# Performance work log

Hardware: AMD Instinct MI355X
Metric: run time of the kernel (lower is better)

The kernel has to match this reference:

```python
import jax, jax.numpy as jnp
import numpy as np

N = 100000
HEADS = 1
DIM = 64
NEG_SLOPE = 0.2


def gat_layer(x, src, dst, W, a_src, a_dst, b):
    # x: [N, F_in]; src/dst: [E] (edge j->i: src=j source, dst=i target)
    h = (x @ W).reshape(N, HEADS, DIM)                      # [N,H,D]
    al_s = jnp.sum(h * a_src[None, :, :], axis=-1)          # [N,H]
    al_d = jnp.sum(h * a_dst[None, :, :], axis=-1)          # [N,H]
    e = jax.nn.leaky_relu(al_s[src] + al_d[dst], NEG_SLOPE)  # [E,H]
    # per-destination softmax (scatter softmax)
    m = jax.ops.segment_max(e, dst, num_segments=N)          # [N,H]
    ex = jnp.exp(e - m[dst])
    s = jax.ops.segment_sum(ex, dst, num_segments=N)         # [N,H]
    alpha = ex / s[dst]                                      # [E,H]
    msg = alpha[:, :, None] * h[src]                         # [E,H,D]
    out = jax.ops.segment_sum(msg, dst, num_segments=N)      # [N,H,D]
    return out.reshape(N, HEADS * DIM) + b


def setup_inputs() -> dict:
    key = jax.random.key(0)
    ks = jax.random.split(key, 16)
    E = 1600000
    inp = {
        'x': jax.random.normal(ks[0], (N, 128), dtype=jnp.float32),
        'edge_index': jax.random.randint(ks[1], (2, E), 0, N, dtype=jnp.int64),
    }
    dims_in = [128, 64, 64]
    for i in range(3):
        fi = dims_in[i]
        inp[f'W{i}'] = jax.random.normal(ks[2 + 4 * i], (fi, HEADS * DIM), dtype=jnp.float32) / np.sqrt(fi)
        inp[f'as{i}'] = jax.random.normal(ks[3 + 4 * i], (HEADS, DIM), dtype=jnp.float32) / np.sqrt(DIM)
        inp[f'ad{i}'] = jax.random.normal(ks[4 + 4 * i], (HEADS, DIM), dtype=jnp.float32) / np.sqrt(DIM)
        inp[f'b{i}'] = jnp.zeros((HEADS * DIM,), dtype=jnp.float32)
    return inp


def reference(x, edge_index, W0, as0, ad0, b0, W1, as1, ad1, b1, W2, as2, ad2, b2):
    # add self-loops (PyG GATConv default add_self_loops=True)
    loop = jnp.arange(N, dtype=edge_index.dtype)
    src = jnp.concatenate([edge_index[0], loop])
    dst = jnp.concatenate([edge_index[1], loop])
    x = gat_layer(x, src, dst, W0, as0, ad0, b0)
    x = jax.nn.relu(x)
    x = gat_layer(x, src, dst, W1, as1, ad1, b1)
    x = jax.nn.relu(x)
    x = gat_layer(x, src, dst, W2, as2, ad2, b2)
    return x
```

## Files before the change

### kernel.cpp

```cpp
#include <hip/hip_runtime.h>
#include <hip/hip_fp16.h>
#include <math.h>

#define DIM 64
#define CBSH 9
#define CBSZ (1 << CBSH)
#define CHUNK 4096

__device__ __forceinline__ float leaky(float e) { return e > 0.f ? e : 0.2f * e; }

__global__ __launch_bounds__(256) void k_part_hist(
        const int* __restrict__ ei, int* __restrict__ hist2d,
        int E, int NPB, int NCB) {
    __shared__ int hist[256];
    int blk = blockIdx.x;
    int base = blk * CHUNK;
    int ecnt = min(CHUNK, E - base);
    for (int i = threadIdx.x; i < 256; i += 256) hist[i] = 0;
    __syncthreads();
    for (int i = threadIdx.x; i < ecnt; i += 256)
        atomicAdd(&hist[ei[E + base + i] >> CBSH], 1);
    __syncthreads();
    for (int cb = threadIdx.x; cb < NCB; cb += 256)
        hist2d[cb * NPB + blk] = hist[cb];
}

__global__ __launch_bounds__(512) void k_part_scan(
        int* __restrict__ hist2d, int* __restrict__ btot, int NPB) {
    __shared__ int tmp[512];
    int cb = blockIdx.x;
    int t = threadIdx.x;
    int v = (t < NPB) ? hist2d[cb * NPB + t] : 0;
    tmp[t] = v;
    __syncthreads();
    for (int off = 1; off < 512; off <<= 1) {
        int u = (t >= off) ? tmp[t - off] : 0;
        __syncthreads();
        tmp[t] += u;
        __syncthreads();
    }
    if (t < NPB) hist2d[cb * NPB + t] = tmp[t] - v;
    if (t == NPB - 1) btot[cb] = tmp[t];
}

__global__ __launch_bounds__(256) void k_ebase(
        const int* __restrict__ btot, int* __restrict__ ebase,
        int* __restrict__ row_ptr, int NCB, int n, int E) {
    __shared__ int tmp[256];
    int t = threadIdx.x;
    int v = (t < NCB) ? btot[t] : 0;
    tmp[t] = v;
    __syncthreads();
    for (int off = 1; off < 256; off <<= 1) {
        int u = (t >= off) ? tmp[t - off] : 0;
        __syncthreads();
        tmp[t] += u;
        __syncthreads();
    }
    if (t < NCB) ebase[t] = tmp[t] - v;
    if (t == NCB - 1) ebase[NCB] = tmp[t];
    if (t == 0) row_ptr[n] = E + n;
}

__global__ __launch_bounds__(256) void k_part_scatter(
        const int* __restrict__ ei, const int* __restrict__ hist2d,
        const int* __restrict__ ebase, int* __restrict__ part,
        int E, int NPB, int NCB) {
    __shared__ int gb[256];
    __shared__ int cnt[256];
    int blk = blockIdx.x;
    int base = blk * CHUNK;
    int ecnt = min(CHUNK, E - base);
    for (int i = threadIdx.x; i < NCB; i += 256) {
        gb[i] = ebase[i] + hist2d[i * NPB + blk];
        cnt[i] = 0;
    }
    __syncthreads();
    for (int i = threadIdx.x; i < ecnt; i += 256) {
        int s = ei[base + i];
        int d = ei[E + base + i];
        int cb = d >> CBSH;
        int off = atomicAdd(&cnt[cb], 1);
        part[gb[cb] + off] = (s << CBSH) | (d & (CBSZ - 1));
    }
}

__global__ __launch_bounds__(256) void k_bucket_scatter(
        const int* __restrict__ ebase, const int* __restrict__ part,
        int* __restrict__ row_ptr, int* __restrict__ csr, int n) {
    __shared__ int arr[CBSZ];
    __shared__ int lcur[CBSZ];
    int cb = blockIdx.x;
    int d0 = cb << CBSH;
    int nb = min(CBSZ, n - d0);
    int t = threadIdx.x;
    int ebeg = ebase[cb], eend = ebase[cb + 1];
    arr[t] = 0; arr[t + 256] = 0;
    __syncthreads();
    for (int p = ebeg + t; p < eend; p += 256)
        atomicAdd(&arr[part[p] & (CBSZ - 1)], 1);
    __syncthreads();
    int v0 = (t < nb) ? arr[t] + 1 : 0;
    int v1 = (t + 256 < nb) ? arr[t + 256] + 1 : 0;
    __syncthreads();
    arr[t] = v0; arr[t + 256] = v1;
    __syncthreads();
    for (int off = 1; off < 512; off <<= 1) {
        int a0 = (t >= off) ? arr[t - off] : 0;
        int a1 = (t + 256 >= off) ? arr[t + 256 - off] : 0;
        __syncthreads();
        arr[t] += a0; arr[t + 256] += a1;
        __syncthreads();
    }
    int nbase = ebeg + d0;
    if (t < nb) {
        int rp = nbase + arr[t] - v0;
        row_ptr[d0 + t] = rp;
        csr[rp] = d0 + t;
        lcur[t] = rp + 1;
    }
    if (t + 256 < nb) {
        int rp = nbase + arr[t + 256] - v1;
        row_ptr[d0 + t + 256] = rp;
        csr[rp] = d0 + t + 256;
        lcur[t + 256] = rp + 1;
    }
    __syncthreads();
    for (int p = ebeg + t; p < eend; p += 256) {
        int v = part[p];
        int slot = atomicAdd(&lcur[v & (CBSZ - 1)], 1);
        csr[slot] = v >> CBSH;
    }
}

template <int FIN>
__global__ __launch_bounds__(256, 4) void k_gemm_al(
        const float* __restrict__ x, int do_relu,
        const float* __restrict__ W,
        const float* __restrict__ as_, const float* __restrict__ ad_,
        __half* __restrict__ h, float* __restrict__ als, float* __restrict__ ald,
        int n) {
    constexpr int KT = 64;
    constexpr int BM = 64;
    __shared__ float ws[KT * 64];
    __shared__ float xs[BM * (KT + 1)];

    const int tid = threadIdx.x;
    const int row0 = blockIdx.x * BM;
    const int rt = tid >> 4, ct = tid & 15;
    const int r0 = rt * 4, c0 = ct * 4;

    float acc[4][4];
#pragma unroll
    for (int i = 0; i < 4; ++i)
#pragma unroll
        for (int j = 0; j < 4; ++j) acc[i][j] = 0.f;

    for (int kt = 0; kt < FIN; kt += KT) {
#pragma unroll
        for (int p = 0; p < KT * 16 / 256; ++p) {
            int i = tid + p * 256;
            *reinterpret_cast<float4*>(&ws[i * 4]) =
                *reinterpret_cast<const float4*>(&W[kt * 64 + i * 4]);
        }
#pragma unroll
        for (int p = 0; p < BM * (KT / 4) / 256; ++p) {
            int i = tid + p * 256;
            int r = i >> 4;
            int kq = i & 15;
            int grow = row0 + r;
            float4 v = make_float4(0.f, 0.f, 0.f, 0.f);
            if (grow < n)
                v = *reinterpret_cast<const float4*>(&x[(size_t)grow * FIN + kt + kq * 4]);
            if (do_relu) {
                v.x = fmaxf(v.x, 0.f); v.y = fmaxf(v.y, 0.f);
                v.z = fmaxf(v.z, 0.f); v.w = fmaxf(v.w, 0.f);
            }
            float* dst = &xs[r * (KT + 1) + kq * 4];
            dst[0] = v.x; dst[1] = v.y; dst[2] = v.z; dst[3] = v.w;
        }
        __syncthreads();

#pragma unroll 4
        for (int k = 0; k < KT; ++k) {
            float4 wv = *reinterpret_cast<const float4*>(&ws[k * 64 + c0]);
            float xv0 = xs[(r0 + 0) * (KT + 1) + k];
            float xv1 = xs[(r0 + 1) * (KT + 1) + k];
            float xv2 = xs[(r0 + 2) * (KT + 1) + k];
            float xv3 = xs[(r0 + 3) * (KT + 1) + k];
            acc[0][0] = fmaf(xv0, wv.x, acc[0][0]);
            acc[0][1] = fmaf(xv0, wv.y, acc[0][1]);
            acc[0][2] = fmaf(xv0, wv.z, acc[0][2]);
            acc[0][3] = fmaf(xv0, wv.w, acc[0][3]);
            acc[1][0] = fmaf(xv1, wv.x, acc[1][0]);
            acc[1][1] = fmaf(xv1, wv.y, acc[1][1]);
            acc[1][2] = fmaf(xv1, wv.z, acc[1][2]);
            acc[1][3] = fmaf(xv1, wv.w, acc[1][3]);
            acc[2][0] = fmaf(xv2, wv.x, acc[2][0]);
            acc[2][1] = fmaf(xv2, wv.y, acc[2][1]);
            acc[2][2] = fmaf(xv2, wv.z, acc[2][2]);
            acc[2][3] = fmaf(xv2, wv.w, acc[2][3]);
            acc[3][0] = fmaf(xv3, wv.x, acc[3][0]);
            acc[3][1] = fmaf(xv3, wv.y, acc[3][1]);
            acc[3][2] = fmaf(xv3, wv.z, acc[3][2]);
            acc[3][3] = fmaf(xv3, wv.w, acc[3][3]);
        }
        __syncthreads();
    }

    float4 asv = *reinterpret_cast<const float4*>(&as_[c0]);
    float4 adv = *reinterpret_cast<const float4*>(&ad_[c0]);
#pragma unroll
    for (int i = 0; i < 4; ++i) {
        int grow = row0 + r0 + i;
        if (grow < n) {
            __half2 p0 = __floats2half2_rn(acc[i][0], acc[i][1]);
            __half2 p1 = __floats2half2_rn(acc[i][2], acc[i][3]);
            uint2 pk = make_uint2(*reinterpret_cast<unsigned*>(&p0),
                                  *reinterpret_cast<unsigned*>(&p1));
            *reinterpret_cast<uint2*>(&h[(size_t)grow * 64 + c0]) = pk;
        }
        float ps = acc[i][0] * asv.x + acc[i][1] * asv.y +
                   acc[i][2] * asv.z + acc[i][3] * asv.w;
        float pd = acc[i][0] * adv.x + acc[i][1] * adv.y +
                   acc[i][2] * adv.z + acc[i][3] * adv.w;
#pragma unroll
        for (int off = 1; off < 16; off <<= 1) {
            ps += __shfl_xor(ps, off);
            pd += __shfl_xor(pd, off);
        }
        if (ct == 0 && grow < n) { als[grow] = ps; ald[grow] = pd; }
    }
}

__global__ __launch_bounds__(256) void k_node_aggr(
        const int* __restrict__ row_ptr, const int* __restrict__ csr,
        const float* __restrict__ als, const float* __restrict__ ald,
        const __half* __restrict__ h, const float* __restrict__ bias,
        float* __restrict__ out, int n) {
    int wid = threadIdx.x >> 6, lane = threadIdx.x & 63;
    int node = blockIdx.x * 4 + wid;
    if (node >= n) return;
    int beg = row_ptr[node];
    int deg = row_ptr[node + 1] - beg;
    float adv = ald[node];
    const int g = lane >> 5;
    const int q = lane & 31;
    float m = -INFINITY, ssum = 0.f;
    float accx = 0.f, accy = 0.f;
    for (int c0 = 0; c0 < deg; c0 += 64) {
        int cn = min(64, deg - c0);
        int s_l = 0;
        float e_l = -INFINITY;
        if (lane < cn) {
            s_l = csr[beg + c0 + lane];
            e_l = leaky(als[s_l] + adv);
        }
        float cm = e_l;
#pragma unroll
        for (int off = 32; off; off >>= 1) cm = fmaxf(cm, __shfl_xor(cm, off));
        float mnew = fmaxf(m, cm);
        float sc = __expf(m - mnew);
        float w_l = (lane < cn) ? __expf(e_l - mnew) : 0.f;
        float cs = w_l;
#pragma unroll
        for (int off = 32; off; off >>= 1) cs += __shfl_xor(cs, off);
        ssum = ssum * sc + cs;
        accx *= sc; accy *= sc;
        m = mnew;
        int cn8 = (cn + 7) & ~7;
        for (int j = 0; j < cn8; j += 8) {
            int   s0 = __shfl(s_l, j + g),     s1 = __shfl(s_l, j + 2 + g);
            int   s2 = __shfl(s_l, j + 4 + g), s3 = __shfl(s_l, j + 6 + g);
            float w0 = __shfl(w_l, j + g),     w1 = __shfl(w_l, j + 2 + g);
            float w2 = __shfl(w_l, j + 4 + g), w3 = __shfl(w_l, j + 6 + g);
            __half2 a0 = *reinterpret_cast<const __half2*>(&h[(size_t)s0 * DIM + 2 * q]);
            __half2 a1 = *reinterpret_cast<const __half2*>(&h[(size_t)s1 * DIM + 2 * q]);
            __half2 a2 = *reinterpret_cast<const __half2*>(&h[(size_t)s2 * DIM + 2 * q]);
            __half2 a3 = *reinterpret_cast<const __half2*>(&h[(size_t)s3 * DIM + 2 * q]);
            float2 f0 = __half22float2(a0);
            float2 f1 = __half22float2(a1);
            float2 f2 = __half22float2(a2);
            float2 f3 = __half22float2(a3);
            accx = fmaf(w0, f0.x, accx); accy = fmaf(w0, f0.y, accy);
            accx = fmaf(w1, f1.x, accx); accy = fmaf(w1, f1.y, accy);
            accx = fmaf(w2, f2.x, accx); accy = fmaf(w2, f2.y, accy);
            accx = fmaf(w3, f3.x, accx); accy = fmaf(w3, f3.y, accy);
        }
    }
    accx += __shfl_xor(accx, 32);
    accy += __shfl_xor(accy, 32);
    if (lane < 32) {
        float inv = 1.f / ssum;
        float2 o;
        o.x = accx * inv + bias[2 * q];
        o.y = accy * inv + bias[2 * q + 1];
        *reinterpret_cast<float2*>(&out[(size_t)node * DIM + 2 * q]) = o;
    }
}

extern "C" void kernel_launch(void* const* d_in, const int* in_sizes, int n_in,
                              void* d_out, int out_size, void* d_ws, size_t ws_size,
                              hipStream_t stream) {
    const float* x = (const float*)d_in[0];
    const int* ei = (const int*)d_in[1];
    const int n = out_size / DIM;
    const int E = in_sizes[1] / 2;
    const int total_edges = E + n;
    const int NCB = (n + CBSZ - 1) >> CBSH;
    const int NPB = (E + CHUNK - 1) / CHUNK;

    const float *W[3], *as_[3], *ad_[3], *b[3];
    for (int l = 0; l < 3; ++l) {
        W[l]  = (const float*)d_in[2 + 4 * l];
        as_[l] = (const float*)d_in[3 + 4 * l];
        ad_[l] = (const float*)d_in[4 + 4 * l];
        b[l]  = (const float*)d_in[5 + 4 * l];
    }

    char* ws = (char*)d_ws;
    size_t off = 0;
    auto alloc = [&](size_t bytes) {
        void* p = ws + off;
        off = (off + bytes + 255) & ~(size_t)255;
        return p;
    };
    int* row_ptr  = (int*)alloc((size_t)(n + 1) * 4);
    int* hist2d   = (int*)alloc((size_t)NCB * NPB * 4);
    int* btot     = (int*)alloc(256 * 4);
    int* ebase    = (int*)alloc(257 * 4);
    int* csr      = (int*)alloc((size_t)total_edges * 4);
    int* part     = (int*)alloc((size_t)E * 4);
    __half* h     = (__half*)alloc((size_t)n * DIM * 2);
    float* als    = (float*)alloc((size_t)n * 4);
    float* ald    = (float*)alloc((size_t)n * 4);
    float* buf    = (float*)d_out;

    k_part_hist<<<NPB, 256, 0, stream>>>(ei, hist2d, E, NPB, NCB);
    k_part_scan<<<NCB, 512, 0, stream>>>(hist2d, btot, NPB);
    k_ebase<<<1, 256, 0, stream>>>(btot, ebase, row_ptr, NCB, n, E);
    k_part_scatter<<<NPB, 256, 0, stream>>>(ei, hist2d, ebase, part, E, NPB, NCB);
    k_bucket_scatter<<<NCB, 256, 0, stream>>>(ebase, part, row_ptr, csr, n);

    const int aggr_blocks = (n + 3) / 4;
    const int gemm_blocks = (n + 63) / 64;
    const float* xin = x;
    for (int l = 0; l < 3; ++l) {
        if (l == 0) {
            k_gemm_al<128><<<gemm_blocks, 256, 0, stream>>>(
                xin, 0, W[l], as_[l], ad_[l], h, als, ald, n);
        } else {
            k_gemm_al<64><<<gemm_blocks, 256, 0, stream>>>(
                xin, 1, W[l], as_[l], ad_[l], h, als, ald, n);
        }
        float* dst = (l == 2) ? (float*)d_out : buf;
        k_node_aggr<<<aggr_blocks, 256, 0, stream>>>(row_ptr, csr, als, ald, h, b[l], dst, n);
        xin = buf;
    }
}
```

Before: 277.6 us.

## Map each node to a half-wavefront and drop online softmax max tracking

The aggregation kernel now gives each destination node 32 lanes instead of a full 64-lane wavefront, so each block handles 8 nodes. Edges are processed in chunks of 32, and the final cross-half reduction goes away. This targets lanes left idle on low-degree nodes, since the average in-degree is around 17. The online softmax rescaling (running max, exp rescale) is also removed and exp is applied directly to the logits. That saves shuffles and exps per chunk but risks overflow or precision loss if the attention logits grow large.

```diff
diff --git a/kernel.cpp b/kernel.cpp
--- a/kernel.cpp
+++ b/kernel.cpp
@@ -238,46 +238,39 @@
         const float* __restrict__ als, const float* __restrict__ ald,
         const __half* __restrict__ h, const float* __restrict__ bias,
         float* __restrict__ out, int n) {
-    int wid = threadIdx.x >> 6, lane = threadIdx.x & 63;
-    int node = blockIdx.x * 4 + wid;
+    const int lane = threadIdx.x & 63;
+    const int hw = lane >> 5;
+    const int l = lane & 31;
+    const int node = blockIdx.x * 8 + ((threadIdx.x >> 6) << 1) + hw;
     if (node >= n) return;
     int beg = row_ptr[node];
     int deg = row_ptr[node + 1] - beg;
     float adv = ald[node];
-    const int g = lane >> 5;
-    const int q = lane & 31;
-    float m = -INFINITY, ssum = 0.f;
+    float ssum = 0.f;
     float accx = 0.f, accy = 0.f;
-    for (int c0 = 0; c0 < deg; c0 += 64) {
-        int cn = min(64, deg - c0);
+    const int sbase = hw << 5;
+    for (int c0 = 0; c0 < deg; c0 += 32) {
+        int cn = min(32, deg - c0);
         int s_l = 0;
-        float e_l = -INFINITY;
-        if (lane < cn) {
-            s_l = csr[beg + c0 + lane];
-            e_l = leaky(als[s_l] + adv);
-        }
-        float cm = e_l;
-#pragma unroll
-        for (int off = 32; off; off >>= 1) cm = fmaxf(cm, __shfl_xor(cm, off));
-        float mnew = fmaxf(m, cm);
-        float sc = __expf(m - mnew);
-        float w_l = (lane < cn) ? __expf(e_l - mnew) : 0.f;
+        float w_l = 0.f;
+        if (l < cn) {
+            s_l = csr[beg + c0 + l];
+            w_l = __expf(leaky(als[s_l] + adv));
+        }
         float cs = w_l;
 #pragma unroll
-        for (int off = 32; off; off >>= 1) cs += __shfl_xor(cs, off);
-        ssum = ssum * sc + cs;
-        accx *= sc; accy *= sc;
-        m = mnew;
-        int cn8 = (cn + 7) & ~7;
-        for (int j = 0; j < cn8; j += 8) {
-            int   s0 = __shfl(s_l, j + g),     s1 = __shfl(s_l, j + 2 + g);
-            int   s2 = __shfl(s_l, j + 4 + g), s3 = __shfl(s_l, j + 6 + g);
-            float w0 = __shfl(w_l, j + g),     w1 = __shfl(w_l, j + 2 + g);
-            float w2 = __shfl(w_l, j + 4 + g), w3 = __shfl(w_l, j + 6 + g);
-            __half2 a0 = *reinterpret_cast<const __half2*>(&h[(size_t)s0 * DIM + 2 * q]);
-            __half2 a1 = *reinterpret_cast<const __half2*>(&h[(size_t)s1 * DIM + 2 * q]);
-            __half2 a2 = *reinterpret_cast<const __half2*>(&h[(size_t)s2 * DIM + 2 * q]);
-            __half2 a3 = *reinterpret_cast<const __half2*>(&h[(size_t)s3 * DIM + 2 * q]);
+        for (int off = 16; off; off >>= 1) cs += __shfl_xor(cs, off);
+        ssum += cs;
+        int cn4 = (cn + 3) & ~3;
+        for (int j = 0; j < cn4; j += 4) {
+            int   s0 = __shfl(s_l, sbase + j),     s1 = __shfl(s_l, sbase + j + 1);
+            int   s2 = __shfl(s_l, sbase + j + 2), s3 = __shfl(s_l, sbase + j + 3);
+            float w0 = __shfl(w_l, sbase + j),     w1 = __shfl(w_l, sbase + j + 1);
+            float w2 = __shfl(w_l, sbase + j + 2), w3 = __shfl(w_l, sbase + j + 3);
+            __half2 a0 = *reinterpret_cast<const __half2*>(&h[(size_t)s0 * DIM + 2 * l]);
+            __half2 a1 = *reinterpret_cast<const __half2*>(&h[(size_t)s1 * DIM + 2 * l]);
+            __half2 a2 = *reinterpret_cast<const __half2*>(&h[(size_t)s2 * DIM + 2 * l]);
+            __half2 a3 = *reinterpret_cast<const __half2*>(&h[(size_t)s3 * DIM + 2 * l]);
             float2 f0 = __half22float2(a0);
             float2 f1 = __half22float2(a1);
             float2 f2 = __half22float2(a2);
@@ -288,15 +281,11 @@
             accx = fmaf(w3, f3.x, accx); accy = fmaf(w3, f3.y, accy);
         }
     }
-    accx += __shfl_xor(accx, 32);
-    accy += __shfl_xor(accy, 32);
-    if (lane < 32) {
-        float inv = 1.f / ssum;
-        float2 o;
-        o.x = accx * inv + bias[2 * q];
-        o.y = accy * inv + bias[2 * q + 1];
-        *reinterpret_cast<float2*>(&out[(size_t)node * DIM + 2 * q]) = o;
-    }
+    float inv = 1.f / ssum;
+    float2 o;
+    o.x = accx * inv + bias[2 * l];
+    o.y = accy * inv + bias[2 * l + 1];
+    *reinterpret_cast<float2*>(&out[(size_t)node * DIM + 2 * l]) = o;
 }
 
 extern "C" void kernel_launch(void* const* d_in, const int* in_sizes, int n_in,
@@ -342,7 +331,7 @@
     k_part_scatter<<<NPB, 256, 0, stream>>>(ei, hist2d, ebase, part, E, NPB, NCB);
     k_bucket_scatter<<<NCB, 256, 0, stream>>>(ebase, part, row_ptr, csr, n);
 
-    const int aggr_blocks = (n + 3) / 4;
+    const int aggr_blocks = (n + 7) / 8;
     const int gemm_blocks = (n + 63) / 64;
     const float* xin = x;
     for (int l = 0; l < 3; ++l) {
```

After: 241.9 us. 1.15x faster.
